# Kernel tuning notes

Hardware: AMD Instinct MI355X
Metric: run time of the kernel (lower is better)

Reference implementation:

```python
import jax, jax.numpy as jnp
import numpy as np

EPS = 1e-5
GROUPS = 8

def _bn(x, g, b, axes):
    # training-mode batch norm over `axes`, channel axis = 1
    m = jnp.mean(x, axis=axes, keepdims=True)
    v = jnp.var(x, axis=axes, keepdims=True)
    shp = (1, -1) + (1,) * (x.ndim - 2)
    return (x - m) / jnp.sqrt(v + EPS) * g.reshape(shp) + b.reshape(shp)

def setup_inputs() -> dict:
    key = jax.random.key(0)
    k0, k1, k2 = jax.random.split(key, 3)
    N, C, T, V = 64, 256, 64, 25
    out_planes = 256
    gp = out_planes // GROUPS  # 32
    x = jax.random.normal(k0, (N, C, T, V), jnp.float32)
    w_qkv = jax.random.normal(k1, (2 * out_planes, C), jnp.float32) * np.float32(np.sqrt(1.0 / C))
    relative = jax.random.normal(k2, (2 * gp, 2 * V - 1), jnp.float32) * np.float32(np.sqrt(1.0 / gp))
    return {
        "x": x,
        "w_qkv": w_qkv,
        "relative": relative,
        "bn_qkv_g": jnp.ones(2 * out_planes, jnp.float32),
        "bn_qkv_b": jnp.zeros(2 * out_planes, jnp.float32),
        "bn_sim_g": jnp.ones(3 * GROUPS, jnp.float32),
        "bn_sim_b": jnp.zeros(3 * GROUPS, jnp.float32),
        "bn_out_g": jnp.ones(2 * out_planes, jnp.float32),
        "bn_out_b": jnp.zeros(2 * out_planes, jnp.float32),
    }

def reference(x, w_qkv, relative, bn_qkv_g, bn_qkv_b, bn_sim_g, bn_sim_b, bn_out_g, bn_out_b):
    N, C, T, V = x.shape
    out_planes = w_qkv.shape[0] // 2
    gp = out_planes // GROUPS
    K = V  # kernel_size == V by construction
    # static relative index table
    qi = np.arange(K)[None, :]
    ki = np.arange(K)[:, None]
    flat_idx = (ki - qi + K - 1).reshape(-1)
    # mean over frames T (permute(0,2,1,3) then mean over dim1 == mean over axis 2)
    y = jnp.mean(x, axis=2)  # [N, C, V]
    # 1x1 conv qkv + BN1d
    qkv = _bn(jnp.einsum('oc,ncv->nov', w_qkv, y), bn_qkv_g, bn_qkv_b, (0, 2))
    qkv = qkv.reshape(N, GROUPS, 2 * gp, V)
    q, k, v = qkv[:, :, : gp // 2], qkv[:, :, gp // 2: gp], qkv[:, :, gp:]
    all_emb = relative[:, flat_idx].reshape(2 * gp, K, K)
    q_e, k_e, v_e = all_emb[: gp // 2], all_emb[gp // 2: gp], all_emb[gp:]
    qr = jnp.einsum('ngci,cij->ngij', q, q_e)
    kr = jnp.einsum('ngci,cij->ngij', k, k_e).swapaxes(2, 3)
    qk = jnp.einsum('ngci,ngcj->ngij', q, k)
    stacked = jnp.concatenate([qk, qr, kr], axis=1)  # [N, 3*groups, V, V]
    stacked = _bn(stacked, bn_sim_g, bn_sim_b, (0, 2, 3)).reshape(N, 3, GROUPS, V, V).sum(axis=1)
    sim = jax.nn.softmax(stacked, axis=3)  # [N, groups, V, V]
    sv = jnp.einsum('ngij,ngcj->ngci', sim, v)
    sve = jnp.einsum('ngij,cij->ngci', sim, v_e)
    so = jnp.concatenate([sv, sve], axis=-1).reshape(N, 2 * out_planes, V)
    o = _bn(so, bn_out_g, bn_out_b, (0, 2)).reshape(N, out_planes, 2, V).sum(axis=2)
    o = jax.nn.sigmoid(o)[:, :, None, :]  # [N, out_planes, 1, V]
    return x + x * o
```

## Files before the change

kernel.cpp:

```cpp
#include <hip/hip_runtime.h>
#include <cmath>

#define NN 64
#define CC 256
#define TT 64
#define VV 25
#define OO 512
#define GG 8
#define NV (NN*VV)
#define STK 625

__global__ __launch_bounds__(256) void k_mean(const float* __restrict__ x,
                                              float* __restrict__ y) {
    __shared__ float tile[TT * VV];
    __shared__ float part[8 * VV];
    int b = blockIdx.x;
    int t = threadIdx.x;
    const float4* x4 = (const float4*)(x + (size_t)b * (TT * VV));
    float4* t4 = (float4*)tile;
    for (int i = t; i < (TT * VV) / 4; i += 256) t4[i] = x4[i];
    __syncthreads();
    if (t < 200) {
        int v = t % VV, s = t / VV;
        float a = 0.f;
        #pragma unroll
        for (int k = 0; k < 8; ++k) a += tile[(s * 8 + k) * VV + v];
        part[s * VV + v] = a;
    }
    __syncthreads();
    if (t < VV) {
        float a = 0.f;
        #pragma unroll
        for (int s = 0; s < 8; ++s) a += part[s * VV + t];
        y[(size_t)b * VV + t] = a * (1.0f / TT);
    }
}

__global__ __launch_bounds__(256) void k_gemm(const float* __restrict__ y,
                                              const float* __restrict__ w,
                                              float* __restrict__ qkv,
                                              float* __restrict__ qstat) {
    __shared__ float ys[CC * VV];
    int n = blockIdx.x >> 3, oc = blockIdx.x & 7;
    int t = threadIdx.x;
    const float* yp = y + (size_t)n * CC * VV;
    for (int i = t; i < CC * VV; i += 256) ys[i] = yp[i];
    __syncthreads();
    int v = t % VV, o0 = t / VV;
    int obase = oc * 64 + o0;
    float acc[8] = {0, 0, 0, 0, 0, 0, 0, 0};
    if (t < 200) {
        for (int c = 0; c < CC; c += 4) {
            float y0 = ys[c * VV + v], y1 = ys[(c + 1) * VV + v];
            float y2 = ys[(c + 2) * VV + v], y3 = ys[(c + 3) * VV + v];
            #pragma unroll
            for (int u = 0; u < 8; ++u) {
                const float4 w4 = *(const float4*)&w[(size_t)(obase + u * 8) * CC + c];
                acc[u] += y0 * w4.x + y1 * w4.y + y2 * w4.z + y3 * w4.w;
            }
        }
        #pragma unroll
        for (int u = 0; u < 8; ++u)
            qkv[((size_t)n * OO + obase + u * 8) * VV + v] = acc[u];
    }
    __syncthreads();
    if (t < 200) {
        #pragma unroll
        for (int u = 0; u < 8; ++u) ys[(o0 + 8 * u) * VV + v] = acc[u];
    }
    __syncthreads();
    if (t < 64) {
        float s = 0.f, s2 = 0.f;
        #pragma unroll
        for (int k = 0; k < VV; ++k) { float w0 = ys[t * VV + k]; s += w0; s2 += w0 * w0; }
        int ch = oc * 64 + t;
        atomicAdd(&qstat[2 * ch], s);
        atomicAdd(&qstat[2 * ch + 1], s2);
    }
}

__global__ __launch_bounds__(256) void k_scores(const float* __restrict__ qkv,
                                                const float* __restrict__ rel,
                                                const float* __restrict__ qstat,
                                                const float* __restrict__ gq,
                                                const float* __restrict__ bq,
                                                float* __restrict__ stk,
                                                float* __restrict__ sstat) {
    int n = blockIdx.x >> 3, gidx = blockIdx.x & 7;
    __shared__ float qs[16][VV], ks[16][VV], rs[32][49];
    __shared__ float qscl[32], qshl[32];
    __shared__ float red0[256], red1[256], red2[256];
    int t = threadIdx.x;
    if (t < 32) {
        int o = gidx * 64 + t;
        float s = qstat[2 * o], s2 = qstat[2 * o + 1];
        float m = s * (1.0f / NV), var = s2 * (1.0f / NV) - m * m;
        float sc = gq[o] * rsqrtf(var + 1e-5f);
        qscl[t] = sc; qshl[t] = bq[o] - m * sc;
    }
    __syncthreads();
    for (int i = t; i < 32 * VV; i += 256) {
        int c = i / VV, v = i - c * VV;
        int o = gidx * 64 + c;
        float val = qkv[((size_t)n * OO + o) * VV + v] * qscl[c] + qshl[c];
        if (c < 16) qs[c][v] = val; else ks[c - 16][v] = val;
    }
    for (int i = t; i < 32 * 49; i += 256) rs[i / 49][i % 49] = rel[i];
    __syncthreads();
    float sqk = 0.f, sqr = 0.f, skr = 0.f, sqk2 = 0.f, sqr2 = 0.f, skr2 = 0.f;
    for (int ij = t; ij < STK; ij += 256) {
        int i = ij / VV, j = ij - (ij / VV) * VV;
        float aqk = 0.f, aqr = 0.f, akr = 0.f;
        #pragma unroll
        for (int c = 0; c < 16; ++c) {
            float qv = qs[c][i], kv = ks[c][j];
            aqk += qv * kv;
            aqr += qv * rs[c][i - j + 24];
            akr += kv * rs[16 + c][j - i + 24];
        }
        size_t base = (size_t)n * 24;
        stk[(base + gidx) * STK + ij]      = aqk;
        stk[(base + 8 + gidx) * STK + ij]  = aqr;
        stk[(base + 16 + gidx) * STK + ij] = akr;
        sqk += aqk; sqk2 += aqk * aqk;
        sqr += aqr; sqr2 += aqr * aqr;
        skr += akr; skr2 += akr * akr;
    }
    red0[t] = sqk; red1[t] = sqr; red2[t] = skr;
    __syncthreads();
    for (int off = 128; off > 0; off >>= 1) {
        if (t < off) { red0[t] += red0[t + off]; red1[t] += red1[t + off]; red2[t] += red2[t + off]; }
        __syncthreads();
    }
    if (t == 0) {
        atomicAdd(&sstat[2 * gidx], red0[0]);
        atomicAdd(&sstat[2 * (8 + gidx)], red1[0]);
        atomicAdd(&sstat[2 * (16 + gidx)], red2[0]);
    }
    __syncthreads();
    red0[t] = sqk2; red1[t] = sqr2; red2[t] = skr2;
    __syncthreads();
    for (int off = 128; off > 0; off >>= 1) {
        if (t < off) { red0[t] += red0[t + off]; red1[t] += red1[t + off]; red2[t] += red2[t + off]; }
        __syncthreads();
    }
    if (t == 0) {
        atomicAdd(&sstat[2 * gidx + 1], red0[0]);
        atomicAdd(&sstat[2 * (8 + gidx) + 1], red1[0]);
        atomicAdd(&sstat[2 * (16 + gidx) + 1], red2[0]);
    }
}

__global__ __launch_bounds__(256) void k_attnout(const float* __restrict__ stk,
                                                 const float* __restrict__ qkv,
                                                 const float* __restrict__ rel,
                                                 const float* __restrict__ qstat,
                                                 const float* __restrict__ gq,
                                                 const float* __restrict__ bq,
                                                 const float* __restrict__ sstat,
                                                 const float* __restrict__ gs,
                                                 const float* __restrict__ bs,
                                                 float* __restrict__ so,
                                                 float* __restrict__ ostat) {
    int n = blockIdx.x >> 3, gidx = blockIdx.x & 7;
    __shared__ float S[STK];
    __shared__ float vs[32][VV];
    __shared__ float rs[32][49];
    __shared__ float scratch[64 * VV];
    __shared__ float sscl[3], sshl[3], vscl[32], vshl[32];
    int t = threadIdx.x;
    if (t < 3) {
        int ch = 8 * t + gidx;
        float s = sstat[2 * ch], s2 = sstat[2 * ch + 1];
        const float inv = 1.0f / 40000.0f;
        float m = s * inv, var = s2 * inv - m * m;
        float sc = gs[ch] * rsqrtf(var + 1e-5f);
        sscl[t] = sc; sshl[t] = bs[ch] - m * sc;
    }
    if (t >= 32 && t < 64) {
        int c = t - 32;
        int o = gidx * 64 + 32 + c;
        float s = qstat[2 * o], s2 = qstat[2 * o + 1];
        float m = s * (1.0f / NV), var = s2 * (1.0f / NV) - m * m;
        float sc = gq[o] * rsqrtf(var + 1e-5f);
        vscl[c] = sc; vshl[c] = bq[o] - m * sc;
    }
    __syncthreads();
    const size_t sb = (size_t)n * 24 * STK;
    for (int ij = t; ij < STK; ij += 256) {
        float a = stk[sb + (size_t)gidx * STK + ij] * sscl[0] + sshl[0];
        a += stk[sb + (size_t)(8 + gidx) * STK + ij] * sscl[1] + sshl[1];
        a += stk[sb + (size_t)(16 + gidx) * STK + ij] * sscl[2] + sshl[2];
        S[ij] = a;
    }
    for (int i = t; i < 32 * VV; i += 256) {
        int c = i / VV, v = i - (i / VV) * VV;
        int o = gidx * 64 + 32 + c;
        vs[c][v] = qkv[((size_t)n * OO + o) * VV + v] * vscl[c] + vshl[c];
    }
    for (int i = t; i < 32 * 49; i += 256) rs[i / 49][i % 49] = rel[32 * 49 + i];
    __syncthreads();
    if (t < VV) {
        int i = t;
        float m = -1e30f;
        #pragma unroll
        for (int j = 0; j < VV; ++j) m = fmaxf(m, S[i * VV + j]);
        float sum = 0.f;
        float e[VV];
        #pragma unroll
        for (int j = 0; j < VV; ++j) { e[j] = expf(S[i * VV + j] - m); sum += e[j]; }
        float inv = 1.0f / sum;
        #pragma unroll
        for (int j = 0; j < VV; ++j) S[i * VV + j] = e[j] * inv;
    }
    __syncthreads();
    for (int idx = t; idx < 32 * VV; idx += 256) {
        int c = idx / VV, i = idx - (idx / VV) * VV;
        float sv = 0.f, sve = 0.f;
        #pragma unroll
        for (int j = 0; j < VV; ++j) {
            float p = S[i * VV + j];
            sv  += p * vs[c][j];
            sve += p * rs[c][i - j + 24];
        }
        size_t o = (size_t)(gidx * 32 + c) * 2;
        so[((size_t)n * OO + o) * VV + i]     = sv;
        so[((size_t)n * OO + o + 1) * VV + i] = sve;
        scratch[(2 * c) * VV + i]     = sv;
        scratch[(2 * c + 1) * VV + i] = sve;
    }
    __syncthreads();
    if (t < 64) {
        float s = 0.f, s2 = 0.f;
        #pragma unroll
        for (int k = 0; k < VV; ++k) { float w0 = scratch[t * VV + k]; s += w0; s2 += w0 * w0; }
        int ch = gidx * 64 + t;
        atomicAdd(&ostat[2 * ch], s);
        atomicAdd(&ostat[2 * ch + 1], s2);
    }
}

__global__ __launch_bounds__(256) void k_final(const float* __restrict__ x,
                                               const float* __restrict__ so,
                                               const float* __restrict__ ostat,
                                               const float* __restrict__ go,
                                               const float* __restrict__ bo,
                                               float* __restrict__ out) {
    int b = blockIdx.x;
    int n = b >> 8, p = b & 255;
    int t = threadIdx.x;
    __shared__ float osl[2], oshl[2], orow[VV];
    if (t < 2) {
        int ch = 2 * p + t;
        float s = ostat[2 * ch], s2 = ostat[2 * ch + 1];
        float m = s * (1.0f / NV), var = s2 * (1.0f / NV) - m * m;
        float sc = go[ch] * rsqrtf(var + 1e-5f);
        osl[t] = sc; oshl[t] = bo[ch] - m * sc;
    }
    __syncthreads();
    if (t < VV) {
        int o0 = 2 * p, o1 = 2 * p + 1;
        float a  = so[((size_t)n * OO + o0) * VV + t] * osl[0] + oshl[0];
        float c2 = so[((size_t)n * OO + o1) * VV + t] * osl[1] + oshl[1];
        float z = a + c2;
        orow[t] = 1.0f + 1.0f / (1.0f + expf(-z));
    }
    __syncthreads();
    const float4* x4 = (const float4*)(x + (size_t)b * (TT * VV));
    float4* y4 = (float4*)(out + (size_t)b * (TT * VV));
    for (int wv = t; wv < (TT * VV) / 4; wv += 256) {
        float4 xv = x4[wv];
        int e = 4 * wv;
        int v0 = e % VV;
        float4 r;
        int v;
        v = v0;                      r.x = xv.x * orow[v];
        v = v0 + 1; if (v >= VV) v -= VV; r.y = xv.y * orow[v];
        v = v0 + 2; if (v >= VV) v -= VV; r.z = xv.z * orow[v];
        v = v0 + 3; if (v >= VV) v -= VV; r.w = xv.w * orow[v];
        y4[wv] = r;
    }
}

extern "C" void kernel_launch(void* const* d_in, const int* in_sizes, int n_in,
                              void* d_out, int out_size, void* d_ws, size_t ws_size,
                              hipStream_t stream) {
    (void)in_sizes; (void)n_in; (void)out_size; (void)ws_size;
    const float* x        = (const float*)d_in[0];
    const float* w_qkv    = (const float*)d_in[1];
    const float* relative = (const float*)d_in[2];
    const float* bn_qkv_g = (const float*)d_in[3];
    const float* bn_qkv_b = (const float*)d_in[4];
    const float* bn_sim_g = (const float*)d_in[5];
    const float* bn_sim_b = (const float*)d_in[6];
    const float* bn_out_g = (const float*)d_in[7];
    const float* bn_out_b = (const float*)d_in[8];
    float* out = (float*)d_out;

    float* ws = (float*)d_ws;
    float* w_y    = ws;
    float* w_qkvp = ws + 409600;
    float* w_stk  = ws + 1228800;
    float* w_so   = ws + 2188800;
    float* qstat  = ws + 3008000;
    float* sstat  = qstat + 1024;
    float* ostat  = sstat + 48;
    hipMemsetAsync(qstat, 0, 2096 * sizeof(float), stream);

    k_mean<<<NN * CC, 256, 0, stream>>>(x, w_y);
    k_gemm<<<NN * 8, 256, 0, stream>>>(w_y, w_qkv, w_qkvp, qstat);
    k_scores<<<NN * GG, 256, 0, stream>>>(w_qkvp, relative, qstat, bn_qkv_g, bn_qkv_b, w_stk, sstat);
    k_attnout<<<NN * GG, 256, 0, stream>>>(w_stk, w_qkvp, relative, qstat, bn_qkv_g, bn_qkv_b,
                                           sstat, bn_sim_g, bn_sim_b, w_so, ostat);
    k_final<<<NN * CC, 256, 0, stream>>>(x, w_so, ostat, bn_out_g, bn_out_b, out);
}
```

Baseline: 294.6 us.

## Fuse all stages into one cooperative persistent kernel with grid syncs

Replaces five kernel launches and a memset with a single cooperative kernel of 512 blocks. Stages are separated by grid.sync(), and shared memory is reused through a union. The mean stage now uses strided per-thread column sums instead of tiled block loads, and the final stage handles 32 rows per block. The aim is to remove launch overhead and inter-kernel gaps. In exchange, the mean and final stages run on far fewer blocks, which can reduce memory-level parallelism for the two bandwidth-heavy passes over x.

```diff
diff --git a/kernel.cpp b/kernel.cpp
--- a/kernel.cpp
+++ b/kernel.cpp
@@ -1,5 +1,8 @@
 #include <hip/hip_runtime.h>
+#include <hip/hip_cooperative_groups.h>
 #include <cmath>
+
+namespace cg = cooperative_groups;
 
 #define NN 64
 #define CC 256
@@ -9,276 +12,273 @@
 #define GG 8
 #define NV (NN*VV)
 #define STK 625
-
-__global__ __launch_bounds__(256) void k_mean(const float* __restrict__ x,
-                                              float* __restrict__ y) {
-    __shared__ float tile[TT * VV];
-    __shared__ float part[8 * VV];
-    int b = blockIdx.x;
-    int t = threadIdx.x;
-    const float4* x4 = (const float4*)(x + (size_t)b * (TT * VV));
-    float4* t4 = (float4*)tile;
-    for (int i = t; i < (TT * VV) / 4; i += 256) t4[i] = x4[i];
-    __syncthreads();
-    if (t < 200) {
-        int v = t % VV, s = t / VV;
-        float a = 0.f;
+#define NBLK 512
+#define NTHR 256
+
+union SMem {
+    float gemm_ys[CC * VV];
+    struct {
+        float qs[16][VV], ks[16][VV], rs[32][49];
+        float qscl[32], qshl[32];
+        float red[3][256];
+    } sc;
+    struct {
+        float S[STK], vs[32][VV], rs[32][49], scratch[64 * VV];
+        float sscl[3], sshl[3], vscl[32], vshl[32];
+    } at;
+    struct {
+        float osl[64], oshl[64], orows[32][VV];
+    } fin;
+};
+
+__global__ __launch_bounds__(256, 2) void k_all(
+    const float* __restrict__ x, const float* __restrict__ w,
+    const float* __restrict__ rel,
+    const float* __restrict__ gq, const float* __restrict__ bq,
+    const float* __restrict__ gs, const float* __restrict__ bs,
+    const float* __restrict__ go, const float* __restrict__ bo,
+    float* __restrict__ y, float* __restrict__ qkv,
+    float* __restrict__ stk, float* __restrict__ so,
+    float* __restrict__ qstat, float* __restrict__ sstat, float* __restrict__ ostat,
+    float* __restrict__ out)
+{
+    cg::grid_group grid = cg::this_grid();
+    __shared__ SMem sm;
+    const int t = threadIdx.x;
+    const int b = blockIdx.x;
+
+    if (b == 0) {
+        for (int i = t; i < 2096; i += NTHR) qstat[i] = 0.f;
+    }
+    for (int o = b * NTHR + t; o < 16384 * VV; o += NBLK * NTHR) {
+        int row = o / VV, v = o - VV * row;
+        const float* xr = x + (size_t)row * (TT * VV) + v;
+        float s = 0.f;
         #pragma unroll
-        for (int k = 0; k < 8; ++k) a += tile[(s * 8 + k) * VV + v];
-        part[s * VV + v] = a;
-    }
-    __syncthreads();
-    if (t < VV) {
-        float a = 0.f;
-        #pragma unroll
-        for (int s = 0; s < 8; ++s) a += part[s * VV + t];
-        y[(size_t)b * VV + t] = a * (1.0f / TT);
-    }
-}
-
-__global__ __launch_bounds__(256) void k_gemm(const float* __restrict__ y,
-                                              const float* __restrict__ w,
-                                              float* __restrict__ qkv,
-                                              float* __restrict__ qstat) {
-    __shared__ float ys[CC * VV];
-    int n = blockIdx.x >> 3, oc = blockIdx.x & 7;
-    int t = threadIdx.x;
-    const float* yp = y + (size_t)n * CC * VV;
-    for (int i = t; i < CC * VV; i += 256) ys[i] = yp[i];
-    __syncthreads();
-    int v = t % VV, o0 = t / VV;
-    int obase = oc * 64 + o0;
-    float acc[8] = {0, 0, 0, 0, 0, 0, 0, 0};
-    if (t < 200) {
-        for (int c = 0; c < CC; c += 4) {
-            float y0 = ys[c * VV + v], y1 = ys[(c + 1) * VV + v];
-            float y2 = ys[(c + 2) * VV + v], y3 = ys[(c + 3) * VV + v];
-            #pragma unroll
-            for (int u = 0; u < 8; ++u) {
-                const float4 w4 = *(const float4*)&w[(size_t)(obase + u * 8) * CC + c];
-                acc[u] += y0 * w4.x + y1 * w4.y + y2 * w4.z + y3 * w4.w;
-            }
-        }
-        #pragma unroll
-        for (int u = 0; u < 8; ++u)
-            qkv[((size_t)n * OO + obase + u * 8) * VV + v] = acc[u];
-    }
-    __syncthreads();
-    if (t < 200) {
-        #pragma unroll
-        for (int u = 0; u < 8; ++u) ys[(o0 + 8 * u) * VV + v] = acc[u];
-    }
-    __syncthreads();
-    if (t < 64) {
-        float s = 0.f, s2 = 0.f;
-        #pragma unroll
-        for (int k = 0; k < VV; ++k) { float w0 = ys[t * VV + k]; s += w0; s2 += w0 * w0; }
-        int ch = oc * 64 + t;
-        atomicAdd(&qstat[2 * ch], s);
-        atomicAdd(&qstat[2 * ch + 1], s2);
-    }
-}
-
-__global__ __launch_bounds__(256) void k_scores(const float* __restrict__ qkv,
-                                                const float* __restrict__ rel,
-                                                const float* __restrict__ qstat,
-                                                const float* __restrict__ gq,
-                                                const float* __restrict__ bq,
-                                                float* __restrict__ stk,
-                                                float* __restrict__ sstat) {
-    int n = blockIdx.x >> 3, gidx = blockIdx.x & 7;
-    __shared__ float qs[16][VV], ks[16][VV], rs[32][49];
-    __shared__ float qscl[32], qshl[32];
-    __shared__ float red0[256], red1[256], red2[256];
-    int t = threadIdx.x;
-    if (t < 32) {
-        int o = gidx * 64 + t;
-        float s = qstat[2 * o], s2 = qstat[2 * o + 1];
-        float m = s * (1.0f / NV), var = s2 * (1.0f / NV) - m * m;
-        float sc = gq[o] * rsqrtf(var + 1e-5f);
-        qscl[t] = sc; qshl[t] = bq[o] - m * sc;
-    }
-    __syncthreads();
-    for (int i = t; i < 32 * VV; i += 256) {
-        int c = i / VV, v = i - c * VV;
-        int o = gidx * 64 + c;
-        float val = qkv[((size_t)n * OO + o) * VV + v] * qscl[c] + qshl[c];
-        if (c < 16) qs[c][v] = val; else ks[c - 16][v] = val;
-    }
-    for (int i = t; i < 32 * 49; i += 256) rs[i / 49][i % 49] = rel[i];
-    __syncthreads();
-    float sqk = 0.f, sqr = 0.f, skr = 0.f, sqk2 = 0.f, sqr2 = 0.f, skr2 = 0.f;
-    for (int ij = t; ij < STK; ij += 256) {
-        int i = ij / VV, j = ij - (ij / VV) * VV;
-        float aqk = 0.f, aqr = 0.f, akr = 0.f;
-        #pragma unroll
-        for (int c = 0; c < 16; ++c) {
-            float qv = qs[c][i], kv = ks[c][j];
-            aqk += qv * kv;
-            aqr += qv * rs[c][i - j + 24];
-            akr += kv * rs[16 + c][j - i + 24];
-        }
-        size_t base = (size_t)n * 24;
-        stk[(base + gidx) * STK + ij]      = aqk;
-        stk[(base + 8 + gidx) * STK + ij]  = aqr;
-        stk[(base + 16 + gidx) * STK + ij] = akr;
-        sqk += aqk; sqk2 += aqk * aqk;
-        sqr += aqr; sqr2 += aqr * aqr;
-        skr += akr; skr2 += akr * akr;
-    }
-    red0[t] = sqk; red1[t] = sqr; red2[t] = skr;
-    __syncthreads();
-    for (int off = 128; off > 0; off >>= 1) {
-        if (t < off) { red0[t] += red0[t + off]; red1[t] += red1[t + off]; red2[t] += red2[t + off]; }
-        __syncthreads();
-    }
-    if (t == 0) {
-        atomicAdd(&sstat[2 * gidx], red0[0]);
-        atomicAdd(&sstat[2 * (8 + gidx)], red1[0]);
-        atomicAdd(&sstat[2 * (16 + gidx)], red2[0]);
-    }
-    __syncthreads();
-    red0[t] = sqk2; red1[t] = sqr2; red2[t] = skr2;
-    __syncthreads();
-    for (int off = 128; off > 0; off >>= 1) {
-        if (t < off) { red0[t] += red0[t + off]; red1[t] += red1[t + off]; red2[t] += red2[t + off]; }
-        __syncthreads();
-    }
-    if (t == 0) {
-        atomicAdd(&sstat[2 * gidx + 1], red0[0]);
-        atomicAdd(&sstat[2 * (8 + gidx) + 1], red1[0]);
-        atomicAdd(&sstat[2 * (16 + gidx) + 1], red2[0]);
-    }
-}
-
-__global__ __launch_bounds__(256) void k_attnout(const float* __restrict__ stk,
-                                                 const float* __restrict__ qkv,
-                                                 const float* __restrict__ rel,
-                                                 const float* __restrict__ qstat,
-                                                 const float* __restrict__ gq,
-                                                 const float* __restrict__ bq,
-                                                 const float* __restrict__ sstat,
-                                                 const float* __restrict__ gs,
-                                                 const float* __restrict__ bs,
-                                                 float* __restrict__ so,
-                                                 float* __restrict__ ostat) {
-    int n = blockIdx.x >> 3, gidx = blockIdx.x & 7;
-    __shared__ float S[STK];
-    __shared__ float vs[32][VV];
-    __shared__ float rs[32][49];
-    __shared__ float scratch[64 * VV];
-    __shared__ float sscl[3], sshl[3], vscl[32], vshl[32];
-    int t = threadIdx.x;
-    if (t < 3) {
-        int ch = 8 * t + gidx;
-        float s = sstat[2 * ch], s2 = sstat[2 * ch + 1];
-        const float inv = 1.0f / 40000.0f;
-        float m = s * inv, var = s2 * inv - m * m;
-        float sc = gs[ch] * rsqrtf(var + 1e-5f);
-        sscl[t] = sc; sshl[t] = bs[ch] - m * sc;
-    }
-    if (t >= 32 && t < 64) {
-        int c = t - 32;
-        int o = gidx * 64 + 32 + c;
-        float s = qstat[2 * o], s2 = qstat[2 * o + 1];
-        float m = s * (1.0f / NV), var = s2 * (1.0f / NV) - m * m;
-        float sc = gq[o] * rsqrtf(var + 1e-5f);
-        vscl[c] = sc; vshl[c] = bq[o] - m * sc;
-    }
-    __syncthreads();
-    const size_t sb = (size_t)n * 24 * STK;
-    for (int ij = t; ij < STK; ij += 256) {
-        float a = stk[sb + (size_t)gidx * STK + ij] * sscl[0] + sshl[0];
-        a += stk[sb + (size_t)(8 + gidx) * STK + ij] * sscl[1] + sshl[1];
-        a += stk[sb + (size_t)(16 + gidx) * STK + ij] * sscl[2] + sshl[2];
-        S[ij] = a;
-    }
-    for (int i = t; i < 32 * VV; i += 256) {
-        int c = i / VV, v = i - (i / VV) * VV;
-        int o = gidx * 64 + 32 + c;
-        vs[c][v] = qkv[((size_t)n * OO + o) * VV + v] * vscl[c] + vshl[c];
-    }
-    for (int i = t; i < 32 * 49; i += 256) rs[i / 49][i % 49] = rel[32 * 49 + i];
-    __syncthreads();
-    if (t < VV) {
-        int i = t;
-        float m = -1e30f;
-        #pragma unroll
-        for (int j = 0; j < VV; ++j) m = fmaxf(m, S[i * VV + j]);
-        float sum = 0.f;
-        float e[VV];
-        #pragma unroll
-        for (int j = 0; j < VV; ++j) { e[j] = expf(S[i * VV + j] - m); sum += e[j]; }
-        float inv = 1.0f / sum;
-        #pragma unroll
-        for (int j = 0; j < VV; ++j) S[i * VV + j] = e[j] * inv;
-    }
-    __syncthreads();
-    for (int idx = t; idx < 32 * VV; idx += 256) {
-        int c = idx / VV, i = idx - (idx / VV) * VV;
-        float sv = 0.f, sve = 0.f;
-        #pragma unroll
-        for (int j = 0; j < VV; ++j) {
-            float p = S[i * VV + j];
-            sv  += p * vs[c][j];
-            sve += p * rs[c][i - j + 24];
-        }
-        size_t o = (size_t)(gidx * 32 + c) * 2;
-        so[((size_t)n * OO + o) * VV + i]     = sv;
-        so[((size_t)n * OO + o + 1) * VV + i] = sve;
-        scratch[(2 * c) * VV + i]     = sv;
-        scratch[(2 * c + 1) * VV + i] = sve;
-    }
-    __syncthreads();
-    if (t < 64) {
-        float s = 0.f, s2 = 0.f;
-        #pragma unroll
-        for (int k = 0; k < VV; ++k) { float w0 = scratch[t * VV + k]; s += w0; s2 += w0 * w0; }
-        int ch = gidx * 64 + t;
-        atomicAdd(&ostat[2 * ch], s);
-        atomicAdd(&ostat[2 * ch + 1], s2);
-    }
-}
-
-__global__ __launch_bounds__(256) void k_final(const float* __restrict__ x,
-                                               const float* __restrict__ so,
-                                               const float* __restrict__ ostat,
-                                               const float* __restrict__ go,
-                                               const float* __restrict__ bo,
-                                               float* __restrict__ out) {
-    int b = blockIdx.x;
-    int n = b >> 8, p = b & 255;
-    int t = threadIdx.x;
-    __shared__ float osl[2], oshl[2], orow[VV];
-    if (t < 2) {
-        int ch = 2 * p + t;
-        float s = ostat[2 * ch], s2 = ostat[2 * ch + 1];
-        float m = s * (1.0f / NV), var = s2 * (1.0f / NV) - m * m;
-        float sc = go[ch] * rsqrtf(var + 1e-5f);
-        osl[t] = sc; oshl[t] = bo[ch] - m * sc;
-    }
-    __syncthreads();
-    if (t < VV) {
-        int o0 = 2 * p, o1 = 2 * p + 1;
-        float a  = so[((size_t)n * OO + o0) * VV + t] * osl[0] + oshl[0];
-        float c2 = so[((size_t)n * OO + o1) * VV + t] * osl[1] + oshl[1];
-        float z = a + c2;
-        orow[t] = 1.0f + 1.0f / (1.0f + expf(-z));
-    }
-    __syncthreads();
-    const float4* x4 = (const float4*)(x + (size_t)b * (TT * VV));
-    float4* y4 = (float4*)(out + (size_t)b * (TT * VV));
-    for (int wv = t; wv < (TT * VV) / 4; wv += 256) {
-        float4 xv = x4[wv];
-        int e = 4 * wv;
-        int v0 = e % VV;
-        float4 r;
-        int v;
-        v = v0;                      r.x = xv.x * orow[v];
-        v = v0 + 1; if (v >= VV) v -= VV; r.y = xv.y * orow[v];
-        v = v0 + 2; if (v >= VV) v -= VV; r.z = xv.z * orow[v];
-        v = v0 + 3; if (v >= VV) v -= VV; r.w = xv.w * orow[v];
-        y4[wv] = r;
+        for (int tt = 0; tt < TT; ++tt) s += xr[tt * VV];
+        y[o] = s * (1.0f / TT);
+    }
+    grid.sync();
+
+    {
+        int n = b >> 3, oc = b & 7;
+        const float* yp = y + (size_t)n * CC * VV;
+        for (int i = t; i < CC * VV; i += NTHR) sm.gemm_ys[i] = yp[i];
+        __syncthreads();
+        int v = t % VV, o0 = t / VV;
+        int obase = oc * 64 + o0;
+        float acc[8] = {0, 0, 0, 0, 0, 0, 0, 0};
+        if (t < 200) {
+            for (int c = 0; c < CC; c += 4) {
+                float y0 = sm.gemm_ys[c * VV + v],       y1 = sm.gemm_ys[(c + 1) * VV + v];
+                float y2 = sm.gemm_ys[(c + 2) * VV + v], y3 = sm.gemm_ys[(c + 3) * VV + v];
+                #pragma unroll
+                for (int u = 0; u < 8; ++u) {
+                    const float4 w4 = *(const float4*)&w[(size_t)(obase + u * 8) * CC + c];
+                    acc[u] += y0 * w4.x + y1 * w4.y + y2 * w4.z + y3 * w4.w;
+                }
+            }
+            #pragma unroll
+            for (int u = 0; u < 8; ++u)
+                qkv[((size_t)n * OO + obase + u * 8) * VV + v] = acc[u];
+        }
+        __syncthreads();
+        if (t < 200) {
+            #pragma unroll
+            for (int u = 0; u < 8; ++u) sm.gemm_ys[(o0 + 8 * u) * VV + v] = acc[u];
+        }
+        __syncthreads();
+        if (t < 64) {
+            float s = 0.f, s2 = 0.f;
+            #pragma unroll
+            for (int k2 = 0; k2 < VV; ++k2) { float w0 = sm.gemm_ys[t * VV + k2]; s += w0; s2 += w0 * w0; }
+            int ch = oc * 64 + t;
+            atomicAdd(&qstat[2 * ch], s);
+            atomicAdd(&qstat[2 * ch + 1], s2);
+        }
+    }
+    grid.sync();
+
+    {
+        int n = b >> 3, gidx = b & 7;
+        if (t < 32) {
+            int o = gidx * 64 + t;
+            float s = qstat[2 * o], s2 = qstat[2 * o + 1];
+            float m = s * (1.0f / NV), var = s2 * (1.0f / NV) - m * m;
+            float sc = gq[o] * rsqrtf(var + 1e-5f);
+            sm.sc.qscl[t] = sc; sm.sc.qshl[t] = bq[o] - m * sc;
+        }
+        __syncthreads();
+        for (int i = t; i < 32 * VV; i += NTHR) {
+            int c = i / VV, v = i - c * VV;
+            int o = gidx * 64 + c;
+            float val = qkv[((size_t)n * OO + o) * VV + v] * sm.sc.qscl[c] + sm.sc.qshl[c];
+            if (c < 16) sm.sc.qs[c][v] = val; else sm.sc.ks[c - 16][v] = val;
+        }
+        for (int i = t; i < 32 * 49; i += NTHR) sm.sc.rs[i / 49][i % 49] = rel[i];
+        __syncthreads();
+        float sqk = 0.f, sqr = 0.f, skr = 0.f, sqk2 = 0.f, sqr2 = 0.f, skr2 = 0.f;
+        for (int ij = t; ij < STK; ij += NTHR) {
+            int i = ij / VV, j = ij - (ij / VV) * VV;
+            float aqk = 0.f, aqr = 0.f, akr = 0.f;
+            #pragma unroll
+            for (int c = 0; c < 16; ++c) {
+                float qv = sm.sc.qs[c][i], kv = sm.sc.ks[c][j];
+                aqk += qv * kv;
+                aqr += qv * sm.sc.rs[c][i - j + 24];
+                akr += kv * sm.sc.rs[16 + c][j - i + 24];
+            }
+            size_t base = (size_t)n * 24;
+            stk[(base + gidx) * STK + ij]      = aqk;
+            stk[(base + 8 + gidx) * STK + ij]  = aqr;
+            stk[(base + 16 + gidx) * STK + ij] = akr;
+            sqk += aqk; sqk2 += aqk * aqk;
+            sqr += aqr; sqr2 += aqr * aqr;
+            skr += akr; skr2 += akr * akr;
+        }
+        sm.sc.red[0][t] = sqk; sm.sc.red[1][t] = sqr; sm.sc.red[2][t] = skr;
+        __syncthreads();
+        for (int off = 128; off > 0; off >>= 1) {
+            if (t < off) {
+                sm.sc.red[0][t] += sm.sc.red[0][t + off];
+                sm.sc.red[1][t] += sm.sc.red[1][t + off];
+                sm.sc.red[2][t] += sm.sc.red[2][t + off];
+            }
+            __syncthreads();
+        }
+        if (t == 0) {
+            atomicAdd(&sstat[2 * gidx], sm.sc.red[0][0]);
+            atomicAdd(&sstat[2 * (8 + gidx)], sm.sc.red[1][0]);
+            atomicAdd(&sstat[2 * (16 + gidx)], sm.sc.red[2][0]);
+        }
+        __syncthreads();
+        sm.sc.red[0][t] = sqk2; sm.sc.red[1][t] = sqr2; sm.sc.red[2][t] = skr2;
+        __syncthreads();
+        for (int off = 128; off > 0; off >>= 1) {
+            if (t < off) {
+                sm.sc.red[0][t] += sm.sc.red[0][t + off];
+                sm.sc.red[1][t] += sm.sc.red[1][t + off];
+                sm.sc.red[2][t] += sm.sc.red[2][t + off];
+            }
+            __syncthreads();
+        }
+        if (t == 0) {
+            atomicAdd(&sstat[2 * gidx + 1], sm.sc.red[0][0]);
+            atomicAdd(&sstat[2 * (8 + gidx) + 1], sm.sc.red[1][0]);
+            atomicAdd(&sstat[2 * (16 + gidx) + 1], sm.sc.red[2][0]);
+        }
+    }
+    grid.sync();
+
+    {
+        int n = b >> 3, gidx = b & 7;
+        if (t < 3) {
+            int ch = 8 * t + gidx;
+            float s = sstat[2 * ch], s2 = sstat[2 * ch + 1];
+            const float inv = 1.0f / 40000.0f;
+            float m = s * inv, var = s2 * inv - m * m;
+            float sc = gs[ch] * rsqrtf(var + 1e-5f);
+            sm.at.sscl[t] = sc; sm.at.sshl[t] = bs[ch] - m * sc;
+        }
+        if (t >= 32 && t < 64) {
+            int c = t - 32;
+            int o = gidx * 64 + 32 + c;
+            float s = qstat[2 * o], s2 = qstat[2 * o + 1];
+            float m = s * (1.0f / NV), var = s2 * (1.0f / NV) - m * m;
+            float sc = gq[o] * rsqrtf(var + 1e-5f);
+            sm.at.vscl[c] = sc; sm.at.vshl[c] = bq[o] - m * sc;
+        }
+        __syncthreads();
+        const size_t sb = (size_t)n * 24 * STK;
+        for (int ij = t; ij < STK; ij += NTHR) {
+            float a = stk[sb + (size_t)gidx * STK + ij] * sm.at.sscl[0] + sm.at.sshl[0];
+            a += stk[sb + (size_t)(8 + gidx) * STK + ij] * sm.at.sscl[1] + sm.at.sshl[1];
+            a += stk[sb + (size_t)(16 + gidx) * STK + ij] * sm.at.sscl[2] + sm.at.sshl[2];
+            sm.at.S[ij] = a;
+        }
+        for (int i = t; i < 32 * VV; i += NTHR) {
+            int c = i / VV, v = i - (i / VV) * VV;
+            int o = gidx * 64 + 32 + c;
+            sm.at.vs[c][v] = qkv[((size_t)n * OO + o) * VV + v] * sm.at.vscl[c] + sm.at.vshl[c];
+        }
+        for (int i = t; i < 32 * 49; i += NTHR) sm.at.rs[i / 49][i % 49] = rel[32 * 49 + i];
+        __syncthreads();
+        if (t < VV) {
+            int i = t;
+            float m = -1e30f;
+            #pragma unroll
+            for (int j = 0; j < VV; ++j) m = fmaxf(m, sm.at.S[i * VV + j]);
+            float sum = 0.f;
+            float e[VV];
+            #pragma unroll
+            for (int j = 0; j < VV; ++j) { e[j] = expf(sm.at.S[i * VV + j] - m); sum += e[j]; }
+            float inv = 1.0f / sum;
+            #pragma unroll
+            for (int j = 0; j < VV; ++j) sm.at.S[i * VV + j] = e[j] * inv;
+        }
+        __syncthreads();
+        for (int idx = t; idx < 32 * VV; idx += NTHR) {
+            int c = idx / VV, i = idx - (idx / VV) * VV;
+            float sv = 0.f, sve = 0.f;
+            #pragma unroll
+            for (int j = 0; j < VV; ++j) {
+                float p = sm.at.S[i * VV + j];
+                sv  += p * sm.at.vs[c][j];
+                sve += p * sm.at.rs[c][i - j + 24];
+            }
+            size_t o = (size_t)(gidx * 32 + c) * 2;
+            so[((size_t)n * OO + o) * VV + i]     = sv;
+            so[((size_t)n * OO + o + 1) * VV + i] = sve;
+            sm.at.scratch[(2 * c) * VV + i]     = sv;
+            sm.at.scratch[(2 * c + 1) * VV + i] = sve;
+        }
+        __syncthreads();
+        if (t < 64) {
+            float s = 0.f, s2 = 0.f;
+            #pragma unroll
+            for (int k2 = 0; k2 < VV; ++k2) { float w0 = sm.at.scratch[t * VV + k2]; s += w0; s2 += w0 * w0; }
+            int ch = gidx * 64 + t;
+            atomicAdd(&ostat[2 * ch], s);
+            atomicAdd(&ostat[2 * ch + 1], s2);
+        }
+    }
+    grid.sync();
+
+    {
+        int row0 = b * 32;
+        int n = row0 >> 8;
+        int p0 = row0 & 255;
+        if (t < 64) {
+            int r = t >> 1, half = t & 1;
+            int ch = 2 * (p0 + r) + half;
+            float s = ostat[2 * ch], s2 = ostat[2 * ch + 1];
+            float m = s * (1.0f / NV), var = s2 * (1.0f / NV) - m * m;
+            float scv = go[ch] * rsqrtf(var + 1e-5f);
+            sm.fin.osl[t] = scv; sm.fin.oshl[t] = bo[ch] - m * scv;
+        }
+        __syncthreads();
+        for (int i = t; i < 32 * VV; i += NTHR) {
+            int r = i / VV, v = i - VV * r;
+            int p = p0 + r;
+            const float* sop = so + ((size_t)n * OO + 2 * p) * VV + v;
+            float a  = sop[0]  * sm.fin.osl[2 * r]     + sm.fin.oshl[2 * r];
+            float b2 = sop[VV] * sm.fin.osl[2 * r + 1] + sm.fin.oshl[2 * r + 1];
+            float z = a + b2;
+            sm.fin.orows[r][v] = 1.0f + 1.0f / (1.0f + expf(-z));
+        }
+        __syncthreads();
+        const float4* x4 = (const float4*)(x + (size_t)row0 * (TT * VV));
+        float4* o4 = (float4*)(out + (size_t)row0 * (TT * VV));
+        for (int i = t; i < 32 * 400; i += NTHR) {
+            int r = i / 400; int e = (i - 400 * r) * 4; int v0 = e % VV;
+            float4 xv = x4[i]; float4 rr;
+            int v;
+            v = v0;                       rr.x = xv.x * sm.fin.orows[r][v];
+            v = v0 + 1; if (v >= VV) v -= VV; rr.y = xv.y * sm.fin.orows[r][v];
+            v = v0 + 2; if (v >= VV) v -= VV; rr.z = xv.z * sm.fin.orows[r][v];
+            v = v0 + 3; if (v >= VV) v -= VV; rr.w = xv.w * sm.fin.orows[r][v];
+            o4[i] = rr;
+        }
     }
 }
 
@@ -305,12 +305,16 @@
     float* qstat  = ws + 3008000;
     float* sstat  = qstat + 1024;
     float* ostat  = sstat + 48;
-    hipMemsetAsync(qstat, 0, 2096 * sizeof(float), stream);
-
-    k_mean<<<NN * CC, 256, 0, stream>>>(x, w_y);
-    k_gemm<<<NN * 8, 256, 0, stream>>>(w_y, w_qkv, w_qkvp, qstat);
-    k_scores<<<NN * GG, 256, 0, stream>>>(w_qkvp, relative, qstat, bn_qkv_g, bn_qkv_b, w_stk, sstat);
-    k_attnout<<<NN * GG, 256, 0, stream>>>(w_stk, w_qkvp, relative, qstat, bn_qkv_g, bn_qkv_b,
-                                           sstat, bn_sim_g, bn_sim_b, w_so, ostat);
-    k_final<<<NN * CC, 256, 0, stream>>>(x, w_so, ostat, bn_out_g, bn_out_b, out);
+
+    void* args[] = {
+        (void*)&x, (void*)&w_qkv, (void*)&relative,
+        (void*)&bn_qkv_g, (void*)&bn_qkv_b,
+        (void*)&bn_sim_g, (void*)&bn_sim_b,
+        (void*)&bn_out_g, (void*)&bn_out_b,
+        (void*)&w_y, (void*)&w_qkvp, (void*)&w_stk, (void*)&w_so,
+        (void*)&qstat, (void*)&sstat, (void*)&ostat,
+        (void*)&out
+    };
+    hipLaunchCooperativeKernel(reinterpret_cast<void*>(k_all),
+                               dim3(NBLK), dim3(NTHR), args, 0, stream);
 }
```

Result: slower. 551.5 us (+87.2%).
